# Optimization experiments

Measured on AMD Instinct MI355X. Metric: run time of the kernel, lower is better.

Reference implementation:

```python
import jax, jax.numpy as jnp
import numpy as np

LAMBD = 0.01  # sparsity_threshold

def softshrink(v, lambd):
    return jnp.sign(v) * jnp.maximum(jnp.abs(v) - lambd, 0.0)

def spectral_gating(y, w1, b1, w2, b2):
    # y: [B, C, H2, W2] float32
    B, C, H2, W2 = y.shape
    nb, bs = w1.shape[1], w1.shape[2]
    f = jnp.fft.rfft2(y, axes=(2, 3), norm='ortho')  # [B, C, H2, W2//2+1] complex64
    Hh, Wf = f.shape[2], f.shape[3]
    xb = f.reshape(B, nb, bs, Hh, Wf)
    xr, xi = xb.real, xb.imag
    # layer 1 (complex block-diagonal matmul, no activation in original)
    o1r = jnp.einsum('bkihw,kio->bkohw', xr, w1[0]) - jnp.einsum('bkihw,kio->bkohw', xi, w1[1]) + b1[0][None, :, :, None, None]
    o1i = jnp.einsum('bkihw,kio->bkohw', xi, w1[0]) + jnp.einsum('bkihw,kio->bkohw', xr, w1[1]) + b1[1][None, :, :, None, None]
    # layer 2
    o2r = jnp.einsum('bkihw,kio->bkohw', o1r, w2[0]) - jnp.einsum('bkihw,kio->bkohw', o1i, w2[1]) + b2[0][None, :, :, None, None]
    o2i = jnp.einsum('bkihw,kio->bkohw', o1i, w2[0]) + jnp.einsum('bkihw,kio->bkohw', o1r, w2[1]) + b2[1][None, :, :, None, None]
    o2r = softshrink(o2r, LAMBD)
    o2i = softshrink(o2i, LAMBD)
    g = (o2r + 1j * o2i).reshape(B, C, Hh, Wf)
    z = g * f  # spectral gating by original FFT
    out = jnp.fft.irfft2(z, s=(H2, W2), axes=(2, 3), norm='ortho')
    return out + y  # residual inside SpectralGatingNetwork

def reference(x, w1, b1, w2, b2):
    B, C, H, W = x.shape
    bias = x
    # max_pool2d(2,2) + avg_pool2d(2,2)
    xr = x.reshape(B, C, H // 2, 2, W // 2, 2)
    y = xr.max(axis=(3, 5)) + xr.mean(axis=(3, 5))  # [B, C, H/2, W/2]
    y = spectral_gating(y, w1, b1, w2, b2)
    # bilinear upsample, align_corners=False (half-pixel centers, same as jax.image.resize)
    y = jax.image.resize(y, (B, C, H, W), method='bilinear')
    return y + bias

def setup_inputs() -> dict:
    key = jax.random.key(0)
    ks = jax.random.split(key, 5)
    B, C, H, W = 8, 128, 256, 256
    nb, bs = 8, 16
    scale = 0.02
    return {
        'x': jax.random.normal(ks[0], (B, C, H, W), dtype=jnp.float32),
        'w1': scale * jax.random.normal(ks[1], (2, nb, bs, bs), dtype=jnp.float32),
        'b1': scale * jax.random.normal(ks[2], (2, nb, bs), dtype=jnp.float32),
        'w2': scale * jax.random.normal(ks[3], (2, nb, bs, bs), dtype=jnp.float32),
        'b2': scale * jax.random.normal(ks[4], (2, nb, bs), dtype=jnp.float32),
    }
```

## Files before the change

### kernel.cpp

```cpp
#include <hip/hip_runtime.h>
#include <math.h>

typedef __attribute__((ext_vector_type(2))) float f2;

#define LPITCH 33
#define LAMBD 0.01f

__device__ __forceinline__ int brev7(int n) { return (int)(__brev((unsigned)n) >> 25); }

__device__ __forceinline__ f2 cmulF(f2 a, f2 w) {
    return (f2){ a.x*w.x - a.y*w.y, a.x*w.y + a.y*w.x };
}
__device__ __forceinline__ f2 cmulC(f2 a, f2 w) {
    return (f2){ a.x*w.x + a.y*w.y, a.y*w.x - a.x*w.y };
}

__device__ __forceinline__ void tw_init(f2* TW, int tid) {
    if (tid < 64) {
        float sv, cv;
        sincosf(-6.283185307179586f * (float)tid / 128.0f, &sv, &cv);
        TW[tid] = (f2){cv, sv};
    }
}

template <bool CONJ>
__device__ __forceinline__ f2 twmul(f2 a, f2 w) { return CONJ ? cmulC(a, w) : cmulF(a, w); }

template <bool CONJ>
__device__ __forceinline__ void dif_passA(f2* S, const f2* TW, int tid) {
    int cw = tid & 31, t = tid >> 5;
    #pragma unroll
    for (int gi = 0; gi < 4; ++gi) {
        int p = t * 4 + gi;
        f2* s0 = S + (size_t)p * LPITCH + cw;
        f2 a = s0[0], b = s0[32*LPITCH], c = s0[64*LPITCH], d = s0[96*LPITCH];
        f2 t0 = a - c, t1 = b - d;
        a = a + c; b = b + d;
        c = twmul<CONJ>(t0, TW[p]);
        d = twmul<CONJ>(t1, TW[p + 32]);
        f2 w6 = TW[2 * p];
        f2 u0 = a - b, u1 = c - d;
        a = a + b; c = c + d;
        b = twmul<CONJ>(u0, w6);
        d = twmul<CONJ>(u1, w6);
        s0[0] = a; s0[32*LPITCH] = b; s0[64*LPITCH] = c; s0[96*LPITCH] = d;
    }
}

template <bool CONJ>
__device__ __forceinline__ void dif_passB(f2* S, const f2* TW, int tid) {
    int cw = tid & 31, t = tid >> 5;
    #pragma unroll
    for (int gi = 0; gi < 4; ++gi) {
        int idx = t * 4 + gi;
        int g = idx >> 3, j = idx & 7;
        f2* s0 = S + (size_t)(g * 32 + j) * LPITCH + cw;
        f2 a = s0[0], b = s0[8*LPITCH], c = s0[16*LPITCH], d = s0[24*LPITCH];
        f2 t0 = a - c, t1 = b - d;
        a = a + c; b = b + d;
        c = twmul<CONJ>(t0, TW[j << 2]);
        d = twmul<CONJ>(t1, TW[(j + 8) << 2]);
        f2 w4 = TW[j << 3];
        f2 u0 = a - b, u1 = c - d;
        a = a + b; c = c + d;
        b = twmul<CONJ>(u0, w4);
        d = twmul<CONJ>(u1, w4);
        s0[0] = a; s0[8*LPITCH] = b; s0[16*LPITCH] = c; s0[24*LPITCH] = d;
    }
}

template <bool CONJ>
__device__ __forceinline__ void dif_passC(f2* S, const f2* TW, int tid) {
    int cw = tid & 31, t = tid >> 5;
    #pragma unroll
    for (int gi = 0; gi < 2; ++gi) {
        int g = t * 2 + gi;
        f2* s0 = S + (size_t)(g * 8) * LPITCH + cw;
        f2 v[8];
        #pragma unroll
        for (int o = 0; o < 8; ++o) v[o] = s0[o*LPITCH];
        #pragma unroll
        for (int o = 0; o < 4; ++o) {
            f2 d = v[o] - v[o+4];
            v[o] = v[o] + v[o+4];
            v[o+4] = twmul<CONJ>(d, TW[o << 4]);
        }
        #pragma unroll
        for (int h2 = 0; h2 < 8; h2 += 4) {
            #pragma unroll
            for (int o = 0; o < 2; ++o) {
                int i0 = h2 + o;
                f2 d = v[i0] - v[i0+2];
                v[i0] = v[i0] + v[i0+2];
                v[i0+2] = twmul<CONJ>(d, TW[o << 5]);
            }
        }
        #pragma unroll
        for (int e = 0; e < 8; e += 2) {
            f2 d = v[e] - v[e+1];
            v[e] = v[e] + v[e+1];
            v[e+1] = d;
        }
        #pragma unroll
        for (int o = 0; o < 8; ++o) s0[o*LPITCH] = v[o];
    }
}

__device__ __forceinline__ void dit_passC(f2* S, const f2* TW, int tid) {
    int cw = tid & 31, t = tid >> 5;
    #pragma unroll
    for (int gi = 0; gi < 2; ++gi) {
        int g = t * 2 + gi;
        f2* s0 = S + (size_t)(g * 8) * LPITCH + cw;
        f2 v[8];
        #pragma unroll
        for (int o = 0; o < 8; ++o) v[o] = s0[o*LPITCH];
        #pragma unroll
        for (int e = 0; e < 8; e += 2) {
            f2 tt = v[e+1];
            v[e+1] = v[e] - tt;
            v[e]   = v[e] + tt;
        }
        #pragma unroll
        for (int h2 = 0; h2 < 8; h2 += 4) {
            #pragma unroll
            for (int o = 0; o < 2; ++o) {
                int i0 = h2 + o;
                f2 tt = cmulC(v[i0+2], TW[o << 5]);
                v[i0+2] = v[i0] - tt;
                v[i0]   = v[i0] + tt;
            }
        }
        #pragma unroll
        for (int o = 0; o < 4; ++o) {
            f2 tt = cmulC(v[o+4], TW[o << 4]);
            v[o+4] = v[o] - tt;
            v[o]   = v[o] + tt;
        }
        #pragma unroll
        for (int o = 0; o < 8; ++o) s0[o*LPITCH] = v[o];
    }
}

__device__ __forceinline__ void dit_passB(f2* S, const f2* TW, int tid) {
    int cw = tid & 31, t = tid >> 5;
    #pragma unroll
    for (int gi = 0; gi < 4; ++gi) {
        int idx = t * 4 + gi;
        int g = idx >> 3, j = idx & 7;
        f2* s0 = S + (size_t)(g * 32 + j) * LPITCH + cw;
        f2 a = s0[0], b = s0[8*LPITCH], c = s0[16*LPITCH], d = s0[24*LPITCH];
        f2 w4 = TW[j << 3];
        f2 tb = cmulC(b, w4), td = cmulC(d, w4);
        b = a - tb; a = a + tb;
        d = c - td; c = c + td;
        f2 tc = cmulC(c, TW[j << 2]);
        f2 te = cmulC(d, TW[(j + 8) << 2]);
        c = a - tc; a = a + tc;
        d = b - te; b = b + te;
        s0[0] = a; s0[8*LPITCH] = b; s0[16*LPITCH] = c; s0[24*LPITCH] = d;
    }
}

__device__ __forceinline__ void dit_passA(f2* S, const f2* TW, int tid) {
    int cw = tid & 31, t = tid >> 5;
    #pragma unroll
    for (int gi = 0; gi < 4; ++gi) {
        int p = t * 4 + gi;
        f2* s0 = S + (size_t)p * LPITCH + cw;
        f2 a = s0[0], b = s0[32*LPITCH], c = s0[64*LPITCH], d = s0[96*LPITCH];
        f2 w6 = TW[2 * p];
        f2 tb = cmulC(b, w6), td = cmulC(d, w6);
        b = a - tb; a = a + tb;
        d = c - td; c = c + td;
        f2 tc = cmulC(c, TW[p]);
        f2 te = cmulC(d, TW[p + 32]);
        c = a - tc; a = a + tc;
        d = b - te; b = b + te;
        s0[0] = a; s0[32*LPITCH] = b; s0[64*LPITCH] = c; s0[96*LPITCH] = d;
    }
}

__global__ __launch_bounds__(256) void poolfft_kernel(const float* __restrict__ x,
                                                      float* __restrict__ y,
                                                      f2* __restrict__ fg) {
    __shared__ f2 S[128 * LPITCH];
    __shared__ f2 TW[64];
    int tid = threadIdx.x;
    int ht = blockIdx.x, k = blockIdx.y, bb = blockIdx.z;
    tw_init(TW, tid);
    #pragma unroll
    for (int it = 0; it < 8; ++it) {
        int u = tid + it * 256;
        int r = u >> 6, q = u & 63;
        int c16 = r & 15, hh = r >> 4;
        int h = ht * 2 + hh;
        const float* p = x + (((size_t)(bb*128 + k*16 + c16) * 256 + 2*h) * 256 + 4*q);
        float4 a = *(const float4*)p;
        float4 b = *(const float4*)(p + 256);
        float v0 = fmaxf(fmaxf(a.x,a.y), fmaxf(b.x,b.y)) + 0.25f*(a.x+a.y+b.x+b.y);
        float v1 = fmaxf(fmaxf(a.z,a.w), fmaxf(b.z,b.w)) + 0.25f*(a.z+a.w+b.z+b.w);
        *(f2*)(y + ((size_t)(bb*128 + k*16 + c16)*128 + h)*128 + 2*q) = (f2){v0, v1};
        S[(2*q)*LPITCH + r]   = (f2){v0, 0.f};
        S[(2*q+1)*LPITCH + r] = (f2){v1, 0.f};
    }
    __syncthreads();
    dif_passA<false>(S, TW, tid); __syncthreads();
    dif_passB<false>(S, TW, tid); __syncthreads();
    dif_passC<false>(S, TW, tid); __syncthreads();
    const float scale = 1.0f / 128.0f;
    f2* dst = fg + (size_t)((bb*8 + k) * 65) * 2048 + ht * 32;
    #pragma unroll
    for (int it = 0; it < 9; ++it) {
        int u = tid + it * 256;
        if (u < 2080) {
            int w = u >> 5, r = u & 31;
            f2 v = S[brev7(w)*LPITCH + r];
            dst[(size_t)w * 2048 + r] = v * scale;
        }
    }
}

__global__ __launch_bounds__(256) void specfused_kernel(f2* __restrict__ fg,
        const float* __restrict__ w1, const float* __restrict__ b1,
        const float* __restrict__ w2, const float* __restrict__ b2) {
    __shared__ f2 S[128 * LPITCH];
    __shared__ f2 TW[64];
    int tid = threadIdx.x;
    int wg = blockIdx.x, k = blockIdx.y, bb = blockIdx.z;
    int ncol = (wg == 32) ? 1 : 2;
    tw_init(TW, tid);
    f2* q2 = fg + (size_t)((bb*8 + k) * 65 + wg * 2) * 2048;
    #pragma unroll
    for (int it = 0; it < 16; ++it) {
        int u = tid + it * 256;
        int wl = u >> 11, rem = u & 2047;
        int h = rem >> 4, c = rem & 15;
        f2 v = (wl < ncol) ? q2[(size_t)wl * 2048 + rem] : (f2){0.f, 0.f};
        S[h*LPITCH + 2*c + wl] = v;
    }
    __syncthreads();
    dif_passA<false>(S, TW, tid); __syncthreads();
    dif_passB<false>(S, TW, tid); __syncthreads();
    dif_passC<false>(S, TW, tid); __syncthreads();
    {
        const float* w1r = w1 + k*256;       const float* w1i = w1 + 2048 + k*256;
        const float* w2r = w2 + k*256;       const float* w2i = w2 + 2048 + k*256;
        const float* b1r = b1 + k*16;        const float* b1i = b1 + 128 + k*16;
        const float* b2r = b2 + k*16;        const float* b2i = b2 + 128 + k*16;
        int pos = tid >> 1, wl = tid & 1;
        f2* sp = S + pos * LPITCH + wl;
        f2 v[16], o1[16], g[16];
        #pragma unroll
        for (int c = 0; c < 16; ++c) v[c] = sp[2*c];
        #pragma unroll
        for (int o = 0; o < 16; ++o) o1[o] = (f2){b1r[o], b1i[o]};
        #pragma unroll
        for (int c = 0; c < 16; ++c) {
            f2 vc = v[c];
            f2 vs = (f2){-vc.y, vc.x};
            #pragma unroll
            for (int o = 0; o < 16; ++o)
                o1[o] += vc * w1r[c*16+o] + vs * w1i[c*16+o];
        }
        #pragma unroll
        for (int o = 0; o < 16; ++o) g[o] = (f2){b2r[o], b2i[o]};
        #pragma unroll
        for (int c = 0; c < 16; ++c) {
            f2 vc = o1[c];
            f2 vs = (f2){-vc.y, vc.x};
            #pragma unroll
            for (int o = 0; o < 16; ++o)
                g[o] += vc * w2r[c*16+o] + vs * w2i[c*16+o];
        }
        #pragma unroll
        for (int o = 0; o < 16; ++o) {
            f2 gg = g[o];
            float ar = copysignf(fmaxf(fabsf(gg.x) - LAMBD, 0.f), gg.x);
            float ai = copysignf(fmaxf(fabsf(gg.y) - LAMBD, 0.f), gg.y);
            sp[2*o] = cmulF(v[o], (f2){ar, ai});
        }
    }
    __syncthreads();
    dit_passC(S, TW, tid); __syncthreads();
    dit_passB(S, TW, tid); __syncthreads();
    dit_passA(S, TW, tid); __syncthreads();
    const float scale = 1.0f / 128.0f;
    #pragma unroll
    for (int it = 0; it < 16; ++it) {
        int u = tid + it * 256;
        int wl = u >> 11, rem = u & 2047;
        int h = rem >> 4, c = rem & 15;
        if (wl < ncol)
            q2[(size_t)wl * 2048 + rem] = S[h*LPITCH + 2*c + wl] * scale;
    }
}

__global__ __launch_bounds__(256) void rowifft_kernel(const f2* __restrict__ fg,
                                                      float* __restrict__ y) {
    __shared__ f2 S[128 * LPITCH];
    __shared__ f2 TW[64];
    int tid = threadIdx.x;
    int ht = blockIdx.x, k = blockIdx.y, bb = blockIdx.z;
    tw_init(TW, tid);
    const f2* src = fg + (size_t)((bb*8 + k) * 65) * 2048 + ht * 32;
    #pragma unroll
    for (int it = 0; it < 9; ++it) {
        int u = tid + it * 256;
        if (u < 2080) {
            int w = u >> 5, r = u & 31;
            f2 v = src[(size_t)w * 2048 + r];
            S[w*LPITCH + r] = v;
            if (w > 0 && w < 64) S[(128 - w)*LPITCH + r] = (f2){v.x, -v.y};
        }
    }
    __syncthreads();
    dif_passA<true>(S, TW, tid); __syncthreads();
    dif_passB<true>(S, TW, tid); __syncthreads();
    dif_passC<true>(S, TW, tid); __syncthreads();
    #pragma unroll
    for (int it = 0; it < 16; ++it) {
        int u = tid + it * 256;
        int t = u & 127, r = u >> 7;
        int c16 = r & 15, hh = r >> 4;
        int h = ht * 2 + hh;
        size_t off = ((size_t)(bb*128 + k*16 + c16) * 128 + h) * 128 + t;
        y[off] += S[brev7(t)*LPITCH + r].x;
    }
}

__global__ __launch_bounds__(256) void upsample_kernel(const float* __restrict__ s, const float* __restrict__ x,
                                                       float* __restrict__ out) {
    int t4 = blockIdx.x * blockDim.x + threadIdx.x;
    int tJ = t4 & 63;
    int r  = t4 >> 6;
    int I  = r & 255;
    int bc = r >> 8;
    float syf = (float)I * 0.5f - 0.25f;
    int y0 = (int)floorf(syf);
    float fy = syf - (float)y0;
    int y1 = y0 + 1; if (y1 > 127) y1 = 127; if (y0 < 0) y0 = 0;
    int u = 2 * tJ;
    int cm1 = u - 1; if (cm1 < 0) cm1 = 0;
    int cp1 = u + 1; if (cp1 > 127) cp1 = 127;
    int cp2 = u + 2; if (cp2 > 127) cp2 = 127;
    const float* sp = s + (size_t)bc * (128 * 128);
    const float* r0p = sp + y0 * 128;
    const float* r1p = sp + y1 * 128;
    float am1 = r0p[cm1], a0 = r0p[u], ap1 = r0p[cp1], ap2 = r0p[cp2];
    float bm1 = r1p[cm1], b0 = r1p[u], bp1 = r1p[cp1], bp2 = r1p[cp2];
    float rm1 = am1 + fy * (bm1 - am1);
    float rr0 = a0  + fy * (b0  - a0);
    float rp1 = ap1 + fy * (bp1 - ap1);
    float rp2 = ap2 + fy * (bp2 - ap2);
    float4 xv = *(const float4*)(x + (size_t)t4 * 4);
    float4 o;
    o.x = rm1 + 0.75f * (rr0 - rm1) + xv.x;
    o.y = rr0 + 0.25f * (rp1 - rr0) + xv.y;
    o.z = rr0 + 0.75f * (rp1 - rr0) + xv.z;
    o.w = rp1 + 0.25f * (rp2 - rp1) + xv.w;
    *(float4*)(out + (size_t)t4 * 4) = o;
}

extern "C" void kernel_launch(void* const* d_in, const int* in_sizes, int n_in,
                              void* d_out, int out_size, void* d_ws, size_t ws_size,
                              hipStream_t stream) {
    const float* x  = (const float*)d_in[0];
    const float* w1 = (const float*)d_in[1];
    const float* b1 = (const float*)d_in[2];
    const float* w2 = (const float*)d_in[3];
    const float* b2 = (const float*)d_in[4];
    float* out = (float*)d_out;
    float* y   = (float*)d_ws;
    f2*    fg  = (f2*)d_out;

    poolfft_kernel<<<dim3(64, 8, 8), 256, 0, stream>>>(x, y, fg);
    specfused_kernel<<<dim3(33, 8, 8), 256, 0, stream>>>(fg, w1, b1, w2, b2);
    rowifft_kernel<<<dim3(64, 8, 8), 256, 0, stream>>>(fg, y);
    upsample_kernel<<<1024 * 256 * 64 / 256, 256, 0, stream>>>(y, x, out);
}
```

Before: 319.5 us.

## Store intermediates in fp16 and use radix-16x8 register FFT in spectral kernel

Intermediate pooled activations and the frequency-domain buffer are now stored as half precision instead of float32, which halves the global memory traffic between the four kernels. The column FFT in the fused spectral kernel is replaced by a two-stage radix-16 by radix-8 register FFT with hardcoded twiddles, cutting the number of shared-memory passes and barriers. The upsample kernel reads packed half pairs to match the new layout. The cost is lower precision in the intermediates, which could push errors past tolerance.

```diff
diff --git a/kernel.cpp b/kernel.cpp
--- a/kernel.cpp
+++ b/kernel.cpp
@@ -2,6 +2,7 @@
 #include <math.h>
 
 typedef __attribute__((ext_vector_type(2))) float f2;
+typedef __attribute__((ext_vector_type(2))) _Float16 h2;
 
 #define LPITCH 33
 #define LAMBD 0.01f
@@ -13,6 +14,65 @@
 }
 __device__ __forceinline__ f2 cmulC(f2 a, f2 w) {
     return (f2){ a.x*w.x + a.y*w.y, a.y*w.x - a.x*w.y };
+}
+__device__ __forceinline__ h2 tohalf(f2 v) { return (h2){(_Float16)v.x, (_Float16)v.y}; }
+__device__ __forceinline__ f2 tofloat(h2 v) { return (f2){(float)v.x, (float)v.y}; }
+
+#define RC 0.70710678118654752440f
+
+__device__ __forceinline__ f2 mul_mi(f2 a)  { return (f2){ a.y, -a.x}; }
+__device__ __forceinline__ f2 mul_pi(f2 a)  { return (f2){-a.y,  a.x}; }
+__device__ __forceinline__ f2 mul_w81(f2 a) { return (f2){ RC*(a.x+a.y),  RC*(a.y-a.x)}; }
+__device__ __forceinline__ f2 mul_w83(f2 a) { return (f2){ RC*(a.y-a.x), -RC*(a.x+a.y)}; }
+__device__ __forceinline__ f2 mul_w8m1(f2 a){ return (f2){ RC*(a.x-a.y),  RC*(a.x+a.y)}; }
+__device__ __forceinline__ f2 mul_w8m3(f2 a){ return (f2){-RC*(a.x+a.y),  RC*(a.x-a.y)}; }
+
+template <bool INV>
+__device__ __forceinline__ void fft16(f2* v) {
+    constexpr float C8 = 0.92387953251128675613f, S8 = 0.38268343236508977173f;
+    constexpr float WR[8] = {1.f,  C8,  RC,  S8, 0.f, -S8, -RC, -C8};
+    constexpr float WI[8] = {0.f, -S8, -RC, -C8, -1.f, -C8, -RC, -S8};
+    #pragma unroll
+    for (int j = 0; j < 8; ++j) {
+        f2 d = v[j] - v[j+8]; v[j] += v[j+8];
+        f2 w = (f2){WR[j], INV ? -WI[j] : WI[j]};
+        v[j+8] = (j == 0) ? d : cmulF(d, w);
+    }
+    #pragma unroll
+    for (int gg = 0; gg < 16; gg += 8) {
+        #pragma unroll
+        for (int j = 0; j < 4; ++j) {
+            int i = gg + j;
+            f2 d = v[i] - v[i+4]; v[i] += v[i+4];
+            f2 w = (f2){WR[2*j], INV ? -WI[2*j] : WI[2*j]};
+            v[i+4] = (j == 0) ? d : cmulF(d, w);
+        }
+    }
+    #pragma unroll
+    for (int gg = 0; gg < 16; gg += 4) {
+        f2 d0 = v[gg] - v[gg+2];   v[gg]   += v[gg+2]; v[gg+2] = d0;
+        f2 d1 = v[gg+1] - v[gg+3]; v[gg+1] += v[gg+3]; v[gg+3] = INV ? mul_pi(d1) : mul_mi(d1);
+    }
+    #pragma unroll
+    for (int gg = 0; gg < 16; gg += 2) {
+        f2 d = v[gg] - v[gg+1]; v[gg] += v[gg+1]; v[gg+1] = d;
+    }
+}
+
+template <bool INV>
+__device__ __forceinline__ void dft8(f2* g) {
+    f2 d0 = g[0]-g[4]; g[0]+=g[4]; g[4] = d0;
+    f2 d1 = g[1]-g[5]; g[1]+=g[5]; g[5] = INV ? mul_w8m1(d1) : mul_w81(d1);
+    f2 d2 = g[2]-g[6]; g[2]+=g[6]; g[6] = INV ? mul_pi(d2)   : mul_mi(d2);
+    f2 d3 = g[3]-g[7]; g[3]+=g[7]; g[7] = INV ? mul_w8m3(d3) : mul_w83(d3);
+    f2 e0 = g[0]-g[2]; g[0]+=g[2]; g[2] = e0;
+    f2 e1 = g[1]-g[3]; g[1]+=g[3]; g[3] = INV ? mul_pi(e1) : mul_mi(e1);
+    f2 e4 = g[4]-g[6]; g[4]+=g[6]; g[6] = e4;
+    f2 e5 = g[5]-g[7]; g[5]+=g[7]; g[7] = INV ? mul_pi(e5) : mul_mi(e5);
+    f2 f0 = g[0]-g[1]; g[0]+=g[1]; g[1] = f0;
+    f2 f1 = g[2]-g[3]; g[2]+=g[3]; g[3] = f1;
+    f2 f4 = g[4]-g[5]; g[4]+=g[5]; g[5] = f4;
+    f2 f6 = g[6]-g[7]; g[6]+=g[7]; g[7] = f6;
 }
 
 __device__ __forceinline__ void tw_init(f2* TW, int tid) {
@@ -86,10 +146,10 @@
             v[o+4] = twmul<CONJ>(d, TW[o << 4]);
         }
         #pragma unroll
-        for (int h2 = 0; h2 < 8; h2 += 4) {
+        for (int h2i = 0; h2i < 8; h2i += 4) {
             #pragma unroll
             for (int o = 0; o < 2; ++o) {
-                int i0 = h2 + o;
+                int i0 = h2i + o;
                 f2 d = v[i0] - v[i0+2];
                 v[i0] = v[i0] + v[i0+2];
                 v[i0+2] = twmul<CONJ>(d, TW[o << 5]);
@@ -106,84 +166,9 @@
     }
 }
 
-__device__ __forceinline__ void dit_passC(f2* S, const f2* TW, int tid) {
-    int cw = tid & 31, t = tid >> 5;
-    #pragma unroll
-    for (int gi = 0; gi < 2; ++gi) {
-        int g = t * 2 + gi;
-        f2* s0 = S + (size_t)(g * 8) * LPITCH + cw;
-        f2 v[8];
-        #pragma unroll
-        for (int o = 0; o < 8; ++o) v[o] = s0[o*LPITCH];
-        #pragma unroll
-        for (int e = 0; e < 8; e += 2) {
-            f2 tt = v[e+1];
-            v[e+1] = v[e] - tt;
-            v[e]   = v[e] + tt;
-        }
-        #pragma unroll
-        for (int h2 = 0; h2 < 8; h2 += 4) {
-            #pragma unroll
-            for (int o = 0; o < 2; ++o) {
-                int i0 = h2 + o;
-                f2 tt = cmulC(v[i0+2], TW[o << 5]);
-                v[i0+2] = v[i0] - tt;
-                v[i0]   = v[i0] + tt;
-            }
-        }
-        #pragma unroll
-        for (int o = 0; o < 4; ++o) {
-            f2 tt = cmulC(v[o+4], TW[o << 4]);
-            v[o+4] = v[o] - tt;
-            v[o]   = v[o] + tt;
-        }
-        #pragma unroll
-        for (int o = 0; o < 8; ++o) s0[o*LPITCH] = v[o];
-    }
-}
-
-__device__ __forceinline__ void dit_passB(f2* S, const f2* TW, int tid) {
-    int cw = tid & 31, t = tid >> 5;
-    #pragma unroll
-    for (int gi = 0; gi < 4; ++gi) {
-        int idx = t * 4 + gi;
-        int g = idx >> 3, j = idx & 7;
-        f2* s0 = S + (size_t)(g * 32 + j) * LPITCH + cw;
-        f2 a = s0[0], b = s0[8*LPITCH], c = s0[16*LPITCH], d = s0[24*LPITCH];
-        f2 w4 = TW[j << 3];
-        f2 tb = cmulC(b, w4), td = cmulC(d, w4);
-        b = a - tb; a = a + tb;
-        d = c - td; c = c + td;
-        f2 tc = cmulC(c, TW[j << 2]);
-        f2 te = cmulC(d, TW[(j + 8) << 2]);
-        c = a - tc; a = a + tc;
-        d = b - te; b = b + te;
-        s0[0] = a; s0[8*LPITCH] = b; s0[16*LPITCH] = c; s0[24*LPITCH] = d;
-    }
-}
-
-__device__ __forceinline__ void dit_passA(f2* S, const f2* TW, int tid) {
-    int cw = tid & 31, t = tid >> 5;
-    #pragma unroll
-    for (int gi = 0; gi < 4; ++gi) {
-        int p = t * 4 + gi;
-        f2* s0 = S + (size_t)p * LPITCH + cw;
-        f2 a = s0[0], b = s0[32*LPITCH], c = s0[64*LPITCH], d = s0[96*LPITCH];
-        f2 w6 = TW[2 * p];
-        f2 tb = cmulC(b, w6), td = cmulC(d, w6);
-        b = a - tb; a = a + tb;
-        d = c - td; c = c + td;
-        f2 tc = cmulC(c, TW[p]);
-        f2 te = cmulC(d, TW[p + 32]);
-        c = a - tc; a = a + tc;
-        d = b - te; b = b + te;
-        s0[0] = a; s0[32*LPITCH] = b; s0[64*LPITCH] = c; s0[96*LPITCH] = d;
-    }
-}
-
 __global__ __launch_bounds__(256) void poolfft_kernel(const float* __restrict__ x,
-                                                      float* __restrict__ y,
-                                                      f2* __restrict__ fg) {
+                                                      _Float16* __restrict__ yh,
+                                                      h2* __restrict__ fgh) {
     __shared__ f2 S[128 * LPITCH];
     __shared__ f2 TW[64];
     int tid = threadIdx.x;
@@ -200,7 +185,7 @@
         float4 b = *(const float4*)(p + 256);
         float v0 = fmaxf(fmaxf(a.x,a.y), fmaxf(b.x,b.y)) + 0.25f*(a.x+a.y+b.x+b.y);
         float v1 = fmaxf(fmaxf(a.z,a.w), fmaxf(b.z,b.w)) + 0.25f*(a.z+a.w+b.z+b.w);
-        *(f2*)(y + ((size_t)(bb*128 + k*16 + c16)*128 + h)*128 + 2*q) = (f2){v0, v1};
+        *(h2*)(yh + (((size_t)(bb*128 + k*16 + c16)*128 + h)*128 + 2*q)) = (h2){(_Float16)v0, (_Float16)v1};
         S[(2*q)*LPITCH + r]   = (f2){v0, 0.f};
         S[(2*q+1)*LPITCH + r] = (f2){v1, 0.f};
     }
@@ -209,40 +194,75 @@
     dif_passB<false>(S, TW, tid); __syncthreads();
     dif_passC<false>(S, TW, tid); __syncthreads();
     const float scale = 1.0f / 128.0f;
-    f2* dst = fg + (size_t)((bb*8 + k) * 65) * 2048 + ht * 32;
+    h2* dst = fgh + (size_t)((bb*8 + k) * 65) * 2048 + ht * 32;
     #pragma unroll
     for (int it = 0; it < 9; ++it) {
         int u = tid + it * 256;
         if (u < 2080) {
             int w = u >> 5, r = u & 31;
             f2 v = S[brev7(w)*LPITCH + r];
-            dst[(size_t)w * 2048 + r] = v * scale;
-        }
-    }
-}
-
-__global__ __launch_bounds__(256) void specfused_kernel(f2* __restrict__ fg,
+            dst[(size_t)w * 2048 + r] = tohalf(v * scale);
+        }
+    }
+}
+
+__global__ __launch_bounds__(256) void specfused_kernel(h2* __restrict__ fgh,
         const float* __restrict__ w1, const float* __restrict__ b1,
         const float* __restrict__ w2, const float* __restrict__ b2) {
     __shared__ f2 S[128 * LPITCH];
-    __shared__ f2 TW[64];
+    __shared__ f2 TW[128];
     int tid = threadIdx.x;
     int wg = blockIdx.x, k = blockIdx.y, bb = blockIdx.z;
     int ncol = (wg == 32) ? 1 : 2;
-    tw_init(TW, tid);
-    f2* q2 = fg + (size_t)((bb*8 + k) * 65 + wg * 2) * 2048;
+    if (tid < 128) {
+        float sv, cv;
+        sincosf(-6.283185307179586f * (float)tid / 128.0f, &sv, &cv);
+        TW[tid] = (f2){cv, sv};
+    }
+    constexpr int BR4[16] = {0,8,4,12,2,10,6,14,1,9,5,13,3,11,7,15};
+    constexpr int BR3[8]  = {0,4,2,6,1,5,3,7};
+    h2* q2 = fgh + (size_t)((bb*8 + k) * 65 + wg * 2) * 2048;
     #pragma unroll
     for (int it = 0; it < 16; ++it) {
         int u = tid + it * 256;
         int wl = u >> 11, rem = u & 2047;
         int h = rem >> 4, c = rem & 15;
-        f2 v = (wl < ncol) ? q2[(size_t)wl * 2048 + rem] : (f2){0.f, 0.f};
+        f2 v = (wl < ncol) ? tofloat(q2[(size_t)wl*2048 + rem]) : (f2){0.f, 0.f};
         S[h*LPITCH + 2*c + wl] = v;
     }
     __syncthreads();
-    dif_passA<false>(S, TW, tid); __syncthreads();
-    dif_passB<false>(S, TW, tid); __syncthreads();
-    dif_passC<false>(S, TW, tid); __syncthreads();
+    int cw = tid & 31, t = tid >> 5;
+    f2* Scw = S + cw;
+    {
+        f2 v[16];
+        #pragma unroll
+        for (int j = 0; j < 16; ++j) v[j] = Scw[(8*j + t) * LPITCH];
+        fft16<false>(v);
+        #pragma unroll
+        for (int r = 0; r < 16; ++r) {
+            int k1 = BR4[r];
+            Scw[(k1*8 + t) * LPITCH] = cmulF(v[r], TW[t * k1]);
+        }
+    }
+    __syncthreads();
+    {
+        f2 a[8], b[8];
+        int k1a = 2*t, k1b = 2*t + 1;
+        #pragma unroll
+        for (int n2 = 0; n2 < 8; ++n2) {
+            a[n2] = Scw[(k1a*8 + n2) * LPITCH];
+            b[n2] = Scw[(k1b*8 + n2) * LPITCH];
+        }
+        dft8<false>(a); dft8<false>(b);
+        __syncthreads();
+        #pragma unroll
+        for (int r = 0; r < 8; ++r) {
+            int k2 = BR3[r];
+            Scw[(k1a + 16*k2) * LPITCH] = a[r];
+            Scw[(k1b + 16*k2) * LPITCH] = b[r];
+        }
+    }
+    __syncthreads();
     {
         const float* w1r = w1 + k*256;       const float* w1i = w1 + 2048 + k*256;
         const float* w2r = w2 + k*256;       const float* w2i = w2 + 2048 + k*256;
@@ -282,9 +302,34 @@
         }
     }
     __syncthreads();
-    dit_passC(S, TW, tid); __syncthreads();
-    dit_passB(S, TW, tid); __syncthreads();
-    dit_passA(S, TW, tid); __syncthreads();
+    {
+        f2 a[8], b[8];
+        int k1a = 2*t, k1b = 2*t + 1;
+        #pragma unroll
+        for (int k2 = 0; k2 < 8; ++k2) {
+            a[k2] = Scw[(k1a + 16*k2) * LPITCH];
+            b[k2] = Scw[(k1b + 16*k2) * LPITCH];
+        }
+        dft8<true>(a); dft8<true>(b);
+        __syncthreads();
+        #pragma unroll
+        for (int r = 0; r < 8; ++r) {
+            int n2 = BR3[r];
+            Scw[(k1a*8 + n2) * LPITCH] = cmulC(a[r], TW[n2 * k1a]);
+            Scw[(k1b*8 + n2) * LPITCH] = cmulC(b[r], TW[n2 * k1b]);
+        }
+    }
+    __syncthreads();
+    {
+        f2 v[16];
+        #pragma unroll
+        for (int j = 0; j < 16; ++j) v[j] = Scw[(8*j + t) * LPITCH];
+        fft16<true>(v);
+        #pragma unroll
+        for (int r = 0; r < 16; ++r)
+            Scw[(8*BR4[r] + t) * LPITCH] = v[r];
+    }
+    __syncthreads();
     const float scale = 1.0f / 128.0f;
     #pragma unroll
     for (int it = 0; it < 16; ++it) {
@@ -292,24 +337,24 @@
         int wl = u >> 11, rem = u & 2047;
         int h = rem >> 4, c = rem & 15;
         if (wl < ncol)
-            q2[(size_t)wl * 2048 + rem] = S[h*LPITCH + 2*c + wl] * scale;
-    }
-}
-
-__global__ __launch_bounds__(256) void rowifft_kernel(const f2* __restrict__ fg,
-                                                      float* __restrict__ y) {
+            q2[(size_t)wl*2048 + rem] = tohalf(S[h*LPITCH + 2*c + wl] * scale);
+    }
+}
+
+__global__ __launch_bounds__(256) void rowifft_kernel(const h2* __restrict__ fgh,
+                                                      _Float16* __restrict__ yh) {
     __shared__ f2 S[128 * LPITCH];
     __shared__ f2 TW[64];
     int tid = threadIdx.x;
     int ht = blockIdx.x, k = blockIdx.y, bb = blockIdx.z;
     tw_init(TW, tid);
-    const f2* src = fg + (size_t)((bb*8 + k) * 65) * 2048 + ht * 32;
+    const h2* src = fgh + (size_t)((bb*8 + k) * 65) * 2048 + ht * 32;
     #pragma unroll
     for (int it = 0; it < 9; ++it) {
         int u = tid + it * 256;
         if (u < 2080) {
             int w = u >> 5, r = u & 31;
-            f2 v = src[(size_t)w * 2048 + r];
+            f2 v = tofloat(src[(size_t)w * 2048 + r]);
             S[w*LPITCH + r] = v;
             if (w > 0 && w < 64) S[(128 - w)*LPITCH + r] = (f2){v.x, -v.y};
         }
@@ -319,17 +364,23 @@
     dif_passB<true>(S, TW, tid); __syncthreads();
     dif_passC<true>(S, TW, tid); __syncthreads();
     #pragma unroll
-    for (int it = 0; it < 16; ++it) {
-        int u = tid + it * 256;
-        int t = u & 127, r = u >> 7;
+    for (int it = 0; it < 8; ++it) {
+        int u = tid + it * 256;
+        int r = u >> 6, tp = u & 63;
         int c16 = r & 15, hh = r >> 4;
         int h = ht * 2 + hh;
-        size_t off = ((size_t)(bb*128 + k*16 + c16) * 128 + h) * 128 + t;
-        y[off] += S[brev7(t)*LPITCH + r].x;
-    }
-}
-
-__global__ __launch_bounds__(256) void upsample_kernel(const float* __restrict__ s, const float* __restrict__ x,
+        size_t offp = ((size_t)(bb*128 + k*16 + c16) * 128 + h) * 64 + tp;
+        h2* yp = (h2*)yh + offp;
+        h2 old = *yp;
+        int p0 = brev7(2*tp);
+        float s0 = (float)old.x + S[p0*LPITCH + r].x;
+        float s1 = (float)old.y + S[(p0+64)*LPITCH + r].x;
+        *yp = (h2){(_Float16)s0, (_Float16)s1};
+    }
+}
+
+__global__ __launch_bounds__(256) void upsample_kernel(const _Float16* __restrict__ sh,
+                                                       const float* __restrict__ x,
                                                        float* __restrict__ out) {
     int t4 = blockIdx.x * blockDim.x + threadIdx.x;
     int tJ = t4 & 63;
@@ -340,15 +391,18 @@
     int y0 = (int)floorf(syf);
     float fy = syf - (float)y0;
     int y1 = y0 + 1; if (y1 > 127) y1 = 127; if (y0 < 0) y0 = 0;
-    int u = 2 * tJ;
-    int cm1 = u - 1; if (cm1 < 0) cm1 = 0;
-    int cp1 = u + 1; if (cp1 > 127) cp1 = 127;
-    int cp2 = u + 2; if (cp2 > 127) cp2 = 127;
-    const float* sp = s + (size_t)bc * (128 * 128);
-    const float* r0p = sp + y0 * 128;
-    const float* r1p = sp + y1 * 128;
-    float am1 = r0p[cm1], a0 = r0p[u], ap1 = r0p[cp1], ap2 = r0p[cp2];
-    float bm1 = r1p[cm1], b0 = r1p[u], bp1 = r1p[cp1], bp2 = r1p[cp2];
+    const h2* r0 = (const h2*)(sh + ((size_t)bc * 128 + y0) * 128);
+    const h2* r1 = (const h2*)(sh + ((size_t)bc * 128 + y1) * 128);
+    int pm = (tJ == 0)  ? 0  : tJ - 1;
+    int pp = (tJ == 63) ? 63 : tJ + 1;
+    h2 a_m = r0[pm], a_0 = r0[tJ], a_p = r0[pp];
+    h2 b_m = r1[pm], b_0 = r1[tJ], b_p = r1[pp];
+    float am1 = (tJ == 0)  ? (float)a_0.x : (float)a_m.y;
+    float a0  = (float)a_0.x, ap1 = (float)a_0.y;
+    float ap2 = (tJ == 63) ? (float)a_p.y : (float)a_p.x;
+    float bm1 = (tJ == 0)  ? (float)b_0.x : (float)b_m.y;
+    float b0  = (float)b_0.x, bp1 = (float)b_0.y;
+    float bp2 = (tJ == 63) ? (float)b_p.y : (float)b_p.x;
     float rm1 = am1 + fy * (bm1 - am1);
     float rr0 = a0  + fy * (b0  - a0);
     float rp1 = ap1 + fy * (bp1 - ap1);
@@ -370,12 +424,12 @@
     const float* b1 = (const float*)d_in[2];
     const float* w2 = (const float*)d_in[3];
     const float* b2 = (const float*)d_in[4];
-    float* out = (float*)d_out;
-    float* y   = (float*)d_ws;
-    f2*    fg  = (f2*)d_out;
-
-    poolfft_kernel<<<dim3(64, 8, 8), 256, 0, stream>>>(x, y, fg);
-    specfused_kernel<<<dim3(33, 8, 8), 256, 0, stream>>>(fg, w1, b1, w2, b2);
-    rowifft_kernel<<<dim3(64, 8, 8), 256, 0, stream>>>(fg, y);
-    upsample_kernel<<<1024 * 256 * 64 / 256, 256, 0, stream>>>(y, x, out);
-}
+    float*     out = (float*)d_out;
+    _Float16*  yh  = (_Float16*)d_ws;
+    h2*        fgh = (h2*)d_out;
+
+    poolfft_kernel<<<dim3(64, 8, 8), 256, 0, stream>>>(x, yh, fgh);
+    specfused_kernel<<<dim3(33, 8, 8), 256, 0, stream>>>(fgh, w1, b1, w2, b2);
+    rowifft_kernel<<<dim3(64, 8, 8), 256, 0, stream>>>(fgh, yh);
+    upsample_kernel<<<1024 * 256 * 64 / 256, 256, 0, stream>>>(yh, x, out);
+}
```

Measured after the change: 280.2 us. 1.14x faster.
